# Kernel tuning notes

Measured on AMD Instinct MI355X. Metric: run time of the kernel, lower is better.

The kernel has to match this reference:

```python
import jax, jax.numpy as jnp
import numpy as np

N_EMBED = 1024
NUM_HEADS = 16
HEAD_SIZE = 64  # NUM_HEADS * HEAD_SIZE == N_EMBED
BLOCK_SIZE = 2048


def setup_inputs() -> dict:
    key = jax.random.key(0)
    ks = jax.random.split(key, 9)
    s = 1.0 / np.sqrt(N_EMBED)
    batch_x = jax.random.normal(ks[0], (4, BLOCK_SIZE, N_EMBED), dtype=jnp.float32)
    # stacked per-head linear params: weight [H, E, d], bias [H, d]
    Wq = jax.random.uniform(ks[1], (NUM_HEADS, N_EMBED, HEAD_SIZE), jnp.float32, -s, s)
    Wk = jax.random.uniform(ks[2], (NUM_HEADS, N_EMBED, HEAD_SIZE), jnp.float32, -s, s)
    Wv = jax.random.uniform(ks[3], (NUM_HEADS, N_EMBED, HEAD_SIZE), jnp.float32, -s, s)
    bq = jax.random.uniform(ks[4], (NUM_HEADS, HEAD_SIZE), jnp.float32, -s, s)
    bk = jax.random.uniform(ks[5], (NUM_HEADS, HEAD_SIZE), jnp.float32, -s, s)
    bv = jax.random.uniform(ks[6], (NUM_HEADS, HEAD_SIZE), jnp.float32, -s, s)
    Wp = jax.random.uniform(ks[7], (N_EMBED, N_EMBED), jnp.float32, -s, s)
    bp = jax.random.uniform(ks[8], (N_EMBED,), jnp.float32, -s, s)
    return {"batch_x": batch_x, "Wq": Wq, "Wk": Wk, "Wv": Wv,
            "bq": bq, "bk": bk, "bv": bv, "Wp": Wp, "bp": bp}


def reference(batch_x, Wq, Wk, Wv, bq, bk, bv, Wp, bp):
    B, T, E = batch_x.shape
    # per-head projections: [B, H, T, d]
    q = jnp.einsum('bte,hed->bhtd', batch_x, Wq) + bq[None, :, None, :]
    k = jnp.einsum('bte,hed->bhtd', batch_x, Wk) + bk[None, :, None, :]
    v = jnp.einsum('bte,hed->bhtd', batch_x, Wv) + bv[None, :, None, :]
    scale = 1.0 / jnp.sqrt(jnp.asarray(HEAD_SIZE, batch_x.dtype))
    wei = jnp.einsum('bhtd,bhsd->bhts', q, k) * scale  # [B,H,T,T]
    causal = jnp.tril(jnp.ones((T, T), dtype=bool))
    wei = jnp.where(causal, wei, jnp.asarray(-jnp.inf, wei.dtype))
    wei = jax.nn.softmax(wei, axis=-1)
    out = jnp.einsum('bhts,bhsd->bhtd', wei, v)  # [B,H,T,d]
    # concat heads (head order matches torch.cat over ModuleList)
    out = out.transpose(0, 2, 1, 3).reshape(B, T, NUM_HEADS * HEAD_SIZE)
    return out @ Wp + bp
```

## Files before the change

kernel.cpp:

```cpp
#include <hip/hip_runtime.h>
#include <math.h>

#define B_ 4
#define T_ 2048
#define E_ 1024
#define H_ 16
#define D_ 64

typedef __bf16 bf16_t;
typedef bf16_t bf16x8 __attribute__((ext_vector_type(8)));
typedef float  f32x4  __attribute__((ext_vector_type(4)));
typedef float  f32x16 __attribute__((ext_vector_type(16)));
typedef unsigned short u16x4 __attribute__((ext_vector_type(4)));

static __device__ __forceinline__ unsigned short f2bf(float f) {
    bf16_t h = (bf16_t)f;
    return __builtin_bit_cast(unsigned short, h);
}

#define GLD(gp, lp) __builtin_amdgcn_global_load_lds( \
    (const __attribute__((address_space(1))) unsigned int*)(gp), \
    (__attribute__((address_space(3))) unsigned int*)(lp), 16, 0, 0)

__global__ void cast_x_kernel(const float* __restrict__ in, unsigned short* __restrict__ out, int n4) {
    int i = blockIdx.x * blockDim.x + threadIdx.x;
    if (i >= n4) return;
    float4 v = ((const float4*)in)[i];
    ushort4 o;
    o.x = f2bf(v.x); o.y = f2bf(v.y); o.z = f2bf(v.z); o.w = f2bf(v.w);
    ((ushort4*)out)[i] = o;
}

__global__ void tcast_all(const float* __restrict__ Wq, const float* __restrict__ Wk,
                          const float* __restrict__ Wv, const float* __restrict__ Wp,
                          unsigned short* __restrict__ wf, unsigned short* __restrict__ wpt) {
    __shared__ unsigned short Ts[64 * 66];
    const int grp = blockIdx.y >> 4, yy = blockIdx.y & 15;
    const float* in; unsigned short* out; int yA, S;
    if (grp == 3) { in = Wp; out = wpt; yA = 64;    S = 1024; }
    else {
        in = (grp == 0) ? Wq : (grp == 1) ? Wk : Wv;
        out = wf + (size_t)grp * 1024 * 1024; yA = 65536; S = 64;
    }
    const int tid = threadIdx.x;
    const int r = tid >> 2, c4 = tid & 3;
    const float* ip = in + (size_t)yA * yy + (size_t)(blockIdx.x * 64 + r) * S + c4 * 16;
    #pragma unroll
    for (int j = 0; j < 4; ++j) {
        float4 v = *(const float4*)&ip[j * 4];
        Ts[(c4 * 16 + j * 4 + 0) * 66 + r] = f2bf(v.x);
        Ts[(c4 * 16 + j * 4 + 1) * 66 + r] = f2bf(v.y);
        Ts[(c4 * 16 + j * 4 + 2) * 66 + r] = f2bf(v.z);
        Ts[(c4 * 16 + j * 4 + 3) * 66 + r] = f2bf(v.w);
    }
    __syncthreads();
    unsigned short* op = out + (size_t)(yy * 64 + r) * 1024 + blockIdx.x * 64 + c4 * 16;
    #pragma unroll
    for (int j = 0; j < 4; ++j) {
        u16x4 pk;
        #pragma unroll
        for (int m = 0; m < 4; ++m) pk[m] = Ts[r * 66 + c4 * 16 + j * 4 + m];
        *(u16x4*)&op[j * 4] = pk;
    }
}

__global__ __launch_bounds__(256) void qkv_gemm(
    const unsigned short* __restrict__ xb,
    const unsigned short* __restrict__ wf,
    const float* __restrict__ bq, const float* __restrict__ bk, const float* __restrict__ bv,
    unsigned short* __restrict__ qo, unsigned short* __restrict__ ko,
    unsigned short* __restrict__ vt)
{
    __shared__ __align__(16) unsigned short sm[17408];
    unsigned short* As = sm;
    unsigned short* Bs = sm + 8192;

    const int tid = threadIdx.x;
    const int w = tid >> 6, lane = tid & 63, l15 = lane & 15, quad = lane >> 4;
    const int m0 = blockIdx.x * 128;
    const int n0 = blockIdx.y * 128;

    f32x4 acc[2][8];
    #pragma unroll
    for (int s = 0; s < 2; ++s)
        #pragma unroll
        for (int n = 0; n < 8; ++n) acc[s][n] = (f32x4){0.f, 0.f, 0.f, 0.f};

    const unsigned short* Ag = xb + (size_t)(m0 + 32 * w + (lane >> 3)) * 1024 + (lane & 7) * 8;
    const unsigned short* Bg = wf + (size_t)(n0 + 32 * w + (lane >> 3)) * 1024 + (lane & 7) * 8;
    unsigned short* Al = As + (32 * w) * 64;
    unsigned short* Bl = Bs + (32 * w) * 64;

    for (int k0 = 0; k0 < 1024; k0 += 64) {
        __syncthreads();
        #pragma unroll
        for (int j = 0; j < 4; ++j) {
            GLD(Ag + (size_t)(8 * j) * 1024 + k0, Al + (8 * j) * 64);
            GLD(Bg + (size_t)(8 * j) * 1024 + k0, Bl + (8 * j) * 64);
        }
        __syncthreads();
        #pragma unroll
        for (int ks = 0; ks < 2; ++ks) {
            bf16x8 a0 = *(const bf16x8*)&As[(32 * w + l15) * 64 + ks * 32 + quad * 8];
            bf16x8 a1 = *(const bf16x8*)&As[(32 * w + 16 + l15) * 64 + ks * 32 + quad * 8];
            #pragma unroll
            for (int n = 0; n < 8; ++n) {
                bf16x8 b = *(const bf16x8*)&Bs[(16 * n + l15) * 64 + ks * 32 + quad * 8];
                acc[0][n] = __builtin_amdgcn_mfma_f32_16x16x32_bf16(a0, b, acc[0][n], 0, 0, 0);
                acc[1][n] = __builtin_amdgcn_mfma_f32_16x16x32_bf16(a1, b, acc[1][n], 0, 0, 0);
            }
        }
    }

    const int which = n0 >> 10;
    const int nb = n0 & 1023;
    if (which < 2) {
        const float* bias = which ? bk : bq;
        unsigned short* out = which ? ko : qo;
        const float sc = which ? 1.f : 0.125f;
        #pragma unroll
        for (int s = 0; s < 2; ++s)
            #pragma unroll
            for (int n = 0; n < 8; ++n) {
                int colg = nb + 16 * n + l15;
                int h = colg >> 6, d = colg & 63;
                float bi = bias[colg];
                #pragma unroll
                for (int r = 0; r < 4; ++r) {
                    int row = m0 + 32 * w + 16 * s + quad * 4 + r;
                    int b = row >> 11, t = row & 2047;
                    out[(((size_t)b * 16 + h) * 2048 + t) * 64 + d] = f2bf((acc[s][n][r] + bi) * sc);
                }
            }
    } else {
        __syncthreads();
        #pragma unroll
        for (int s = 0; s < 2; ++s)
            #pragma unroll
            for (int n = 0; n < 8; ++n) {
                int colg = nb + 16 * n + l15;
                float bi = bv[colg];
                u16x4 pk;
                #pragma unroll
                for (int r = 0; r < 4; ++r) pk[r] = f2bf(acc[s][n][r] + bi);
                *(u16x4*)&sm[(16 * n + l15) * 136 + 32 * w + 16 * s + quad * 4] = pk;
            }
        __syncthreads();
        const int b = m0 >> 11, t0l = m0 & 2047;
        const int nl = tid >> 1, toff = (tid & 1) * 64;
        const int colg = nb + nl;
        const int h = colg >> 6, d = colg & 63;
        unsigned short* dst = vt + (((size_t)b * 16 + h) * 64 + d) * 2048 + t0l + toff;
        #pragma unroll
        for (int j = 0; j < 8; ++j)
            *(float4*)&dst[j * 8] = *(const float4*)&sm[nl * 136 + toff + j * 8];
    }
}

__global__ __launch_bounds__(256, 3) void attn_kernel(
    const unsigned short* __restrict__ q, const unsigned short* __restrict__ k,
    const unsigned short* __restrict__ vt, unsigned short* __restrict__ att2)
{
    __shared__ __align__(16) unsigned short Ks[64 * 64];
    __shared__ __align__(16) unsigned short Vs[64 * 64];
    __shared__ __align__(16) unsigned short Ps[4][32 * 64];

    const int tid = threadIdx.x;
    const int w = tid >> 6, lane = tid & 63;
    const int l31 = lane & 31, h = lane >> 5;
    const int bh = blockIdx.x;
    const int sw_q = l31 & 7;

    unsigned short* Pw = Ps[w];
    const unsigned short* kb = k  + (size_t)bh * 2048 * 64;
    const unsigned short* vb = vt + (size_t)bh * 64 * 2048;
    const int sr = tid >> 2;
    const int sc0 = tid & 3;
    const int ssw = sr & 7;

    for (int leg = 0; leg < 2; ++leg) {
        const int qtile = leg ? (15 - (int)blockIdx.y) : (int)blockIdx.y;
        const int qb0 = qtile * 128;
        const int qg = qb0 + w * 32 + l31;
        const int qmin = qb0 + w * 32, qmax = qmin + 31;
        const int trips = 2 * qtile + 2;

        bf16x8 fQ[4];
        {
            const unsigned short* qp = q + ((size_t)bh * 2048 + qg) * 64 + h * 8;
            #pragma unroll
            for (int ks = 0; ks < 4; ++ks) fQ[ks] = *(const bf16x8*)&qp[ks * 16];
        }

        f32x16 O[2];
        #pragma unroll
        for (int nt = 0; nt < 2; ++nt)
            #pragma unroll
            for (int i = 0; i < 16; ++i) O[nt][i] = 0.f;
        float lsum = 0.f;

        for (int jt = 0; jt < trips; ++jt) {
            __syncthreads();
            {
                const unsigned short* kg = kb + (size_t)(jt * 64) * 64;
                const unsigned short* vg = vb + jt * 64;
                #pragma unroll
                for (int it = 0; it < 2; ++it) {
                    int ci = sc0 + 4 * it;
                    int sw = ((ci ^ ssw)) * 8;
                    *(float4*)&Ks[sr * 64 + sw] = *(const float4*)&kg[(size_t)sr * 64 + ci * 8];
                    *(float4*)&Vs[sr * 64 + sw] = *(const float4*)&vg[(size_t)sr * 2048 + ci * 8];
                }
            }
            __syncthreads();

            const int key0 = jt * 64;
            if (key0 <= qmax) {
                f32x16 S[2];
                #pragma unroll
                for (int kt = 0; kt < 2; ++kt)
                    #pragma unroll
                    for (int i = 0; i < 16; ++i) S[kt][i] = 0.f;
                __builtin_amdgcn_s_setprio(1);
                #pragma unroll
                for (int kt = 0; kt < 2; ++kt) {
                    const int row = kt * 32 + l31, rs = row & 7;
                    #pragma unroll
                    for (int ks = 0; ks < 4; ++ks) {
                        bf16x8 aK = *(const bf16x8*)&Ks[row * 64 + ((2 * ks + h) ^ rs) * 8];
                        S[kt] = __builtin_amdgcn_mfma_f32_32x32x16_bf16(aK, fQ[ks], S[kt], 0, 0, 0);
                    }
                }
                __builtin_amdgcn_s_setprio(0);

                const bool need_mask = (key0 + 63) > qmin;
                #pragma unroll
                for (int kt = 0; kt < 2; ++kt) {
                    #pragma unroll
                    for (int g = 0; g < 4; ++g) {
                        u16x4 pk;
                        #pragma unroll
                        for (int r = 0; r < 4; ++r) {
                            float p = __expf(S[kt][4 * g + r]);
                            if (need_mask) {
                                int key = key0 + kt * 32 + 8 * g + 4 * h + r;
                                if (key > qg) p = 0.f;
                            }
                            lsum += p;
                            pk[r] = f2bf(p);
                        }
                        *(u16x4*)&Pw[l31 * 64 + ((4 * kt + g) ^ sw_q) * 8 + 4 * h] = pk;
                    }
                }
                __builtin_amdgcn_s_setprio(1);
                #pragma unroll
                for (int ks2 = 0; ks2 < 4; ++ks2) {
                    bf16x8 aP = *(const bf16x8*)&Pw[l31 * 64 + ((2 * ks2 + h) ^ sw_q) * 8];
                    #pragma unroll
                    for (int nt = 0; nt < 2; ++nt) {
                        const int drow = nt * 32 + l31;
                        bf16x8 bV = *(const bf16x8*)&Vs[drow * 64 + ((2 * ks2 + h) ^ (drow & 7)) * 8];
                        O[nt] = __builtin_amdgcn_mfma_f32_32x32x16_bf16(aP, bV, O[nt], 0, 0, 0);
                    }
                }
                __builtin_amdgcn_s_setprio(0);
            }
        }

        lsum += __shfl_xor(lsum, 32);
        const float inv = 1.f / lsum;

        unsigned short* ob = att2 + ((size_t)bh * 2048 + qb0 + w * 32) * 64;
        #pragma unroll
        for (int g = 0; g < 4; ++g)
            #pragma unroll
            for (int r = 0; r < 4; ++r) {
                const int qy = 8 * g + 4 * h + r;
                const float iv = __shfl(inv, qy);
                #pragma unroll
                for (int nt = 0; nt < 2; ++nt)
                    ob[(size_t)qy * 64 + nt * 32 + l31] = f2bf(O[nt][4 * g + r] * iv);
            }
    }
}

__global__ __launch_bounds__(256) void proj_gemm(
    const unsigned short* __restrict__ A,
    const unsigned short* __restrict__ wpt,
    const float* __restrict__ bp,
    float* __restrict__ out)
{
    __shared__ __align__(16) unsigned short sm[16384];
    unsigned short* As = sm;
    unsigned short* Bs = sm + 8192;

    const int tid = threadIdx.x;
    const int w = tid >> 6, lane = tid & 63, l15 = lane & 15, quad = lane >> 4;
    const int m0 = blockIdx.x * 128;
    const int n0 = blockIdx.y * 128;

    f32x4 acc[2][8];
    #pragma unroll
    for (int s = 0; s < 2; ++s)
        #pragma unroll
        for (int n = 0; n < 8; ++n) acc[s][n] = (f32x4){0.f, 0.f, 0.f, 0.f};

    const unsigned short* Ag = A + (size_t)(m0 >> 11) * 16 * 131072
                                 + (size_t)((m0 & 2047) + 32 * w + (lane >> 3)) * 64 + (lane & 7) * 8;
    const unsigned short* Bg = wpt + (size_t)(n0 + 32 * w + (lane >> 3)) * 1024 + (lane & 7) * 8;
    unsigned short* Al = As + (32 * w) * 64;
    unsigned short* Bl = Bs + (32 * w) * 64;

    for (int k0 = 0; k0 < 1024; k0 += 64) {
        __syncthreads();
        const size_t aoff = (size_t)(k0 >> 6) * 131072;
        #pragma unroll
        for (int j = 0; j < 4; ++j) {
            GLD(Ag + aoff + (size_t)(8 * j) * 64, Al + (8 * j) * 64);
            GLD(Bg + (size_t)(8 * j) * 1024 + k0, Bl + (8 * j) * 64);
        }
        __syncthreads();
        #pragma unroll
        for (int ks = 0; ks < 2; ++ks) {
            bf16x8 a0 = *(const bf16x8*)&As[(32 * w + l15) * 64 + ks * 32 + quad * 8];
            bf16x8 a1 = *(const bf16x8*)&As[(32 * w + 16 + l15) * 64 + ks * 32 + quad * 8];
            #pragma unroll
            for (int n = 0; n < 8; ++n) {
                bf16x8 b = *(const bf16x8*)&Bs[(16 * n + l15) * 64 + ks * 32 + quad * 8];
                acc[0][n] = __builtin_amdgcn_mfma_f32_16x16x32_bf16(a0, b, acc[0][n], 0, 0, 0);
                acc[1][n] = __builtin_amdgcn_mfma_f32_16x16x32_bf16(a1, b, acc[1][n], 0, 0, 0);
            }
        }
    }

    #pragma unroll
    for (int s = 0; s < 2; ++s)
        #pragma unroll
        for (int n = 0; n < 8; ++n) {
            float bi = bp[n0 + 16 * n + l15];
            #pragma unroll
            for (int r = 0; r < 4; ++r) {
                int row = m0 + 32 * w + 16 * s + quad * 4 + r;
                out[(size_t)row * 1024 + n0 + 16 * n + l15] = acc[s][n][r] + bi;
            }
        }
}

extern "C" void kernel_launch(void* const* d_in, const int* in_sizes, int n_in,
                              void* d_out, int out_size, void* d_ws, size_t ws_size,
                              hipStream_t stream) {
    const float* x  = (const float*)d_in[0];
    const float* Wq = (const float*)d_in[1];
    const float* Wk = (const float*)d_in[2];
    const float* Wv = (const float*)d_in[3];
    const float* bq = (const float*)d_in[4];
    const float* bk = (const float*)d_in[5];
    const float* bv = (const float*)d_in[6];
    const float* Wp = (const float*)d_in[7];
    const float* bp = (const float*)d_in[8];
    float* out = (float*)d_out;

    const size_t nx = (size_t)B_ * T_ * E_;
    unsigned short* base = (unsigned short*)d_ws;
    unsigned short* xb  = base;
    unsigned short* qb  = xb + nx;
    unsigned short* kb  = qb + nx;
    unsigned short* vtb = kb + nx;
    unsigned short* atb = vtb + nx;
    unsigned short* wf  = atb + nx;
    unsigned short* wpt = wf + 3072 * 1024;

    cast_x_kernel<<<(int)(nx / 4 + 255) / 256, 256, 0, stream>>>(x, xb, (int)(nx / 4));
    tcast_all<<<dim3(16, 64), 256, 0, stream>>>(Wq, Wk, Wv, Wp, wf, wpt);
    qkv_gemm<<<dim3(64, 24), 256, 0, stream>>>(xb, wf, bq, bk, bv, qb, kb, vtb);
    attn_kernel<<<dim3(64, 8), 256, 0, stream>>>(qb, kb, vtb, atb);
    proj_gemm<<<dim3(64, 8), 256, 0, stream>>>(atb, wpt, bp, out);
}
```

Before: 291.4 us.

## Rewrite QKV GEMM as 256x256 double-buffered, swizzled, 8-wave pipelined kernel

Reworks the QKV projection GEMM into 256x256 tiles with 8 waves. Global-to-LDS loads are double buffered so the next K tile is prefetched while MFMAs run. The LDS layout gets an XOR swizzle to avoid bank conflicts, and the MFMA phases are interleaved with barriers and s_setprio. The aim is to raise arithmetic intensity and hide load latency in the largest GEMM. In exchange it uses 128KB of LDS per block, leaves fewer blocks in the grid, and makes the V-transpose epilogue more complex.

```diff
diff --git a/kernel.cpp b/kernel.cpp
--- a/kernel.cpp
+++ b/kernel.cpp
@@ -21,6 +21,9 @@
 #define GLD(gp, lp) __builtin_amdgcn_global_load_lds( \
     (const __attribute__((address_space(1))) unsigned int*)(gp), \
     (__attribute__((address_space(3))) unsigned int*)(lp), 16, 0, 0)
+
+#define BAR() __builtin_amdgcn_s_barrier()
+#define WAIT_LGKM0() asm volatile("s_waitcnt lgkmcnt(0)" ::: "memory")
 
 __global__ void cast_x_kernel(const float* __restrict__ in, unsigned short* __restrict__ out, int n4) {
     int i = blockIdx.x * blockDim.x + threadIdx.x;
@@ -64,96 +67,173 @@
     }
 }
 
-__global__ __launch_bounds__(256) void qkv_gemm(
+__global__ __launch_bounds__(512, 2) void qkv_gemm(
     const unsigned short* __restrict__ xb,
     const unsigned short* __restrict__ wf,
     const float* __restrict__ bq, const float* __restrict__ bk, const float* __restrict__ bv,
     unsigned short* __restrict__ qo, unsigned short* __restrict__ ko,
     unsigned short* __restrict__ vt)
 {
-    __shared__ __align__(16) unsigned short sm[17408];
-    unsigned short* As = sm;
-    unsigned short* Bs = sm + 8192;
+    __shared__ __align__(16) unsigned short sm[65536];
 
     const int tid = threadIdx.x;
-    const int w = tid >> 6, lane = tid & 63, l15 = lane & 15, quad = lane >> 4;
-    const int m0 = blockIdx.x * 128;
-    const int n0 = blockIdx.y * 128;
-
-    f32x4 acc[2][8];
+    const int w = tid >> 6, lane = tid & 63;
+    const int wr = w >> 2, wc = w & 3;
+    const int l15 = lane & 15, quad = lane >> 4, lsw = l15 & 7;
+    const int m0 = blockIdx.x * 256;
+    const int n0 = blockIdx.y * 256;
+
+    f32x4 acc[8][4];
     #pragma unroll
-    for (int s = 0; s < 2; ++s)
-        #pragma unroll
-        for (int n = 0; n < 8; ++n) acc[s][n] = (f32x4){0.f, 0.f, 0.f, 0.f};
-
-    const unsigned short* Ag = xb + (size_t)(m0 + 32 * w + (lane >> 3)) * 1024 + (lane & 7) * 8;
-    const unsigned short* Bg = wf + (size_t)(n0 + 32 * w + (lane >> 3)) * 1024 + (lane & 7) * 8;
-    unsigned short* Al = As + (32 * w) * 64;
-    unsigned short* Bl = Bs + (32 * w) * 64;
-
-    for (int k0 = 0; k0 < 1024; k0 += 64) {
-        __syncthreads();
+    for (int i = 0; i < 8; ++i)
+        #pragma unroll
+        for (int j = 0; j < 4; ++j) acc[i][j] = (f32x4){0.f, 0.f, 0.f, 0.f};
+
+    const int swzE = (((lane & 7) ^ (lane >> 3)) * 8);
+    const unsigned short* Agb = xb + (size_t)(m0 + (lane >> 3)) * 1024 + swzE;
+    const unsigned short* Bgb = wf + (size_t)(n0 + (lane >> 3)) * 1024 + swzE;
+
+    auto stage = [&](int t, int q) {
+        unsigned short* Ad = sm + q * 32768 + w * 512;
+        unsigned short* Bd = Ad + 16384;
+        const unsigned short* Ag = Agb + t * 64;
+        const unsigned short* Bg = Bgb + t * 64;
         #pragma unroll
         for (int j = 0; j < 4; ++j) {
-            GLD(Ag + (size_t)(8 * j) * 1024 + k0, Al + (8 * j) * 64);
-            GLD(Bg + (size_t)(8 * j) * 1024 + k0, Bl + (8 * j) * 64);
-        }
-        __syncthreads();
-        #pragma unroll
-        for (int ks = 0; ks < 2; ++ks) {
-            bf16x8 a0 = *(const bf16x8*)&As[(32 * w + l15) * 64 + ks * 32 + quad * 8];
-            bf16x8 a1 = *(const bf16x8*)&As[(32 * w + 16 + l15) * 64 + ks * 32 + quad * 8];
-            #pragma unroll
-            for (int n = 0; n < 8; ++n) {
-                bf16x8 b = *(const bf16x8*)&Bs[(16 * n + l15) * 64 + ks * 32 + quad * 8];
-                acc[0][n] = __builtin_amdgcn_mfma_f32_16x16x32_bf16(a0, b, acc[0][n], 0, 0, 0);
-                acc[1][n] = __builtin_amdgcn_mfma_f32_16x16x32_bf16(a1, b, acc[1][n], 0, 0, 0);
-            }
-        }
+            GLD(Ag + (size_t)(j * 64 + w * 8) * 1024, Ad + j * 4096);
+            GLD(Bg + (size_t)(j * 64 + w * 8) * 1024, Bd + j * 4096);
+        }
+    };
+    auto rdA = [&](const unsigned short* Ad, int fm, int ks) {
+        return *(const bf16x8*)&Ad[(wr * 128 + fm * 16 + l15) * 64 + (((ks * 4 + quad) ^ lsw) * 8)];
+    };
+    auto rdB = [&](const unsigned short* Bd, int fn, int ks) {
+        return *(const bf16x8*)&Bd[(wc * 64 + fn * 16 + l15) * 64 + (((ks * 4 + quad) ^ lsw) * 8)];
+    };
+
+    stage(0, 0);
+    stage(1, 1);
+    asm volatile("s_waitcnt vmcnt(8)" ::: "memory");
+    BAR();
+
+    for (int T = 0; T < 16; ++T) {
+        const unsigned short* Ad = sm + (T & 1) * 32768;
+        const unsigned short* Bd = Ad + 16384;
+        bf16x8 fA[4][2], fB[4][2];
+
+        #pragma unroll
+        for (int i = 0; i < 4; ++i) { fA[i][0] = rdA(Ad, i, 0); fA[i][1] = rdA(Ad, i, 1); }
+        #pragma unroll
+        for (int j = 0; j < 2; ++j) { fB[j][0] = rdB(Bd, j, 0); fB[j][1] = rdB(Bd, j, 1); }
+        BAR(); WAIT_LGKM0();
+        __builtin_amdgcn_s_setprio(1);
+        #pragma unroll
+        for (int i = 0; i < 4; ++i)
+            #pragma unroll
+            for (int j = 0; j < 2; ++j)
+                #pragma unroll
+                for (int ks = 0; ks < 2; ++ks)
+                    acc[i][j] = __builtin_amdgcn_mfma_f32_16x16x32_bf16(fA[i][ks], fB[j][ks], acc[i][j], 0, 0, 0);
+        __builtin_amdgcn_s_setprio(0);
+        BAR();
+
+        #pragma unroll
+        for (int j = 0; j < 2; ++j) { fB[2 + j][0] = rdB(Bd, 2 + j, 0); fB[2 + j][1] = rdB(Bd, 2 + j, 1); }
+        BAR(); WAIT_LGKM0();
+        __builtin_amdgcn_s_setprio(1);
+        #pragma unroll
+        for (int i = 0; i < 4; ++i)
+            #pragma unroll
+            for (int j = 0; j < 2; ++j)
+                #pragma unroll
+                for (int ks = 0; ks < 2; ++ks)
+                    acc[i][2 + j] = __builtin_amdgcn_mfma_f32_16x16x32_bf16(fA[i][ks], fB[2 + j][ks], acc[i][2 + j], 0, 0, 0);
+        __builtin_amdgcn_s_setprio(0);
+        BAR();
+
+        #pragma unroll
+        for (int i = 0; i < 4; ++i) { fA[i][0] = rdA(Ad, 4 + i, 0); fA[i][1] = rdA(Ad, 4 + i, 1); }
+        BAR(); WAIT_LGKM0();
+        __builtin_amdgcn_s_setprio(1);
+        #pragma unroll
+        for (int i = 0; i < 4; ++i)
+            #pragma unroll
+            for (int j = 0; j < 2; ++j)
+                #pragma unroll
+                for (int ks = 0; ks < 2; ++ks)
+                    acc[4 + i][2 + j] = __builtin_amdgcn_mfma_f32_16x16x32_bf16(fA[i][ks], fB[2 + j][ks], acc[4 + i][2 + j], 0, 0, 0);
+        __builtin_amdgcn_s_setprio(0);
+        BAR();
+
+        if (T < 14) {
+            stage(T + 2, T & 1);
+            asm volatile("s_waitcnt vmcnt(8)" ::: "memory");
+        } else {
+            asm volatile("s_waitcnt vmcnt(0)" ::: "memory");
+        }
+        BAR();
+        __builtin_amdgcn_s_setprio(1);
+        #pragma unroll
+        for (int i = 0; i < 4; ++i)
+            #pragma unroll
+            for (int j = 0; j < 2; ++j)
+                #pragma unroll
+                for (int ks = 0; ks < 2; ++ks)
+                    acc[4 + i][j] = __builtin_amdgcn_mfma_f32_16x16x32_bf16(fA[i][ks], fB[j][ks], acc[4 + i][j], 0, 0, 0);
+        __builtin_amdgcn_s_setprio(0);
+        BAR();
     }
 
     const int which = n0 >> 10;
     const int nb = n0 & 1023;
     if (which < 2) {
         const float* bias = which ? bk : bq;
-        unsigned short* out = which ? ko : qo;
+        unsigned short* outp = which ? ko : qo;
         const float sc = which ? 1.f : 0.125f;
         #pragma unroll
-        for (int s = 0; s < 2; ++s)
-            #pragma unroll
-            for (int n = 0; n < 8; ++n) {
-                int colg = nb + 16 * n + l15;
+        for (int fm = 0; fm < 8; ++fm)
+            #pragma unroll
+            for (int fn = 0; fn < 4; ++fn) {
+                int colg = nb + wc * 64 + fn * 16 + l15;
                 int h = colg >> 6, d = colg & 63;
                 float bi = bias[colg];
                 #pragma unroll
                 for (int r = 0; r < 4; ++r) {
-                    int row = m0 + 32 * w + 16 * s + quad * 4 + r;
+                    int row = m0 + wr * 128 + fm * 16 + quad * 4 + r;
                     int b = row >> 11, t = row & 2047;
-                    out[(((size_t)b * 16 + h) * 2048 + t) * 64 + d] = f2bf((acc[s][n][r] + bi) * sc);
+                    outp[(((size_t)b * 16 + h) * 2048 + t) * 64 + d] = f2bf((acc[fm][fn][r] + bi) * sc);
                 }
             }
     } else {
-        __syncthreads();
-        #pragma unroll
-        for (int s = 0; s < 2; ++s)
-            #pragma unroll
-            for (int n = 0; n < 8; ++n) {
-                int colg = nb + 16 * n + l15;
-                float bi = bv[colg];
-                u16x4 pk;
-                #pragma unroll
-                for (int r = 0; r < 4; ++r) pk[r] = f2bf(acc[s][n][r] + bi);
-                *(u16x4*)&sm[(16 * n + l15) * 136 + 32 * w + 16 * s + quad * 4] = pk;
-            }
-        __syncthreads();
-        const int b = m0 >> 11, t0l = m0 & 2047;
-        const int nl = tid >> 1, toff = (tid & 1) * 64;
-        const int colg = nb + nl;
-        const int h = colg >> 6, d = colg & 63;
-        unsigned short* dst = vt + (((size_t)b * 16 + h) * 64 + d) * 2048 + t0l + toff;
-        #pragma unroll
-        for (int j = 0; j < 8; ++j)
-            *(float4*)&dst[j * 8] = *(const float4*)&sm[nl * 136 + toff + j * 8];
+        const int b = m0 >> 11;
+        for (int mh = 0; mh < 2; ++mh)
+            for (int nh = 0; nh < 2; ++nh) {
+                __syncthreads();
+                if (wr == mh && (wc >> 1) == nh) {
+                    const int cc = wc & 1;
+                    #pragma unroll
+                    for (int fm = 0; fm < 8; ++fm)
+                        #pragma unroll
+                        for (int fn = 0; fn < 4; ++fn) {
+                            int colL = cc * 64 + fn * 16 + l15;
+                            int colg = nb + nh * 128 + colL;
+                            float bi = bv[colg];
+                            u16x4 pk;
+                            #pragma unroll
+                            for (int r = 0; r < 4; ++r) pk[r] = f2bf(acc[fm][fn][r] + bi);
+                            *(u16x4*)&sm[colL * 136 + fm * 16 + quad * 4] = pk;
+                        }
+                }
+                __syncthreads();
+                const int nl = tid >> 2, tq = tid & 3;
+                const int colg = nb + nh * 128 + nl;
+                const int h = colg >> 6, d = colg & 63;
+                const int t0 = (m0 & 2047) + mh * 128;
+                unsigned short* dst = vt + (((size_t)b * 16 + h) * 64 + d) * 2048 + t0 + tq * 32;
+                #pragma unroll
+                for (int j = 0; j < 4; ++j)
+                    *(float4*)&dst[j * 8] = *(const float4*)&sm[nl * 136 + tq * 32 + j * 8];
+            }
     }
 }
 
@@ -372,7 +452,7 @@
 
     cast_x_kernel<<<(int)(nx / 4 + 255) / 256, 256, 0, stream>>>(x, xb, (int)(nx / 4));
     tcast_all<<<dim3(16, 64), 256, 0, stream>>>(Wq, Wk, Wv, Wp, wf, wpt);
-    qkv_gemm<<<dim3(64, 24), 256, 0, stream>>>(xb, wf, bq, bk, bv, qb, kb, vtb);
+    qkv_gemm<<<dim3(32, 12), 512, 0, stream>>>(xb, wf, bq, bk, bv, qb, kb, vtb);
     attn_kernel<<<dim3(64, 8), 256, 0, stream>>>(qb, kb, vtb, atb);
     proj_gemm<<<dim3(64, 8), 256, 0, stream>>>(atb, wpt, bp, out);
 }
```

Result: faster. 282.7 us (-3.0%).
